# Kernel optimization log

Measured on AMD Instinct MI355X. Metric: run time of the kernel, lower is better.

The kernel has to match this reference:

```python
import jax, jax.numpy as jnp
import numpy as np

N_NODES = 50000
N_EDGES = 1600000
IN_DIM = 128
OUT_DIM = 32
N_HEADS = 4


def setup_inputs() -> dict:
    key = jax.random.key(0)
    k_x, k_e, k_w, k_a = jax.random.split(key, 4)
    x = jax.random.normal(k_x, (N_NODES, IN_DIM), dtype=jnp.float32)
    edge_index = jax.random.randint(k_e, (N_EDGES, 2), 0, N_NODES, dtype=jnp.int64)
    # Xavier-uniform-like init scales
    w_bound = np.sqrt(6.0 / (IN_DIM + OUT_DIM)).astype(np.float32)
    a_bound = np.sqrt(6.0 / (N_HEADS + 2 * OUT_DIM)).astype(np.float32)
    weight = jax.random.uniform(k_w, (N_HEADS, IN_DIM, OUT_DIM), dtype=jnp.float32,
                                minval=-w_bound, maxval=w_bound)
    attn = jax.random.uniform(k_a, (N_HEADS, 2 * OUT_DIM), dtype=jnp.float32,
                              minval=-a_bound, maxval=a_bound)
    return {"x": x, "edge_index": edge_index, "weight": weight, "attn": attn}


def reference(x, edge_index, weight, attn):
    # x: [N, in_dim]; edge_index: [E, 2]; weight: [H, in, out]; attn: [H, 2*out]
    num_nodes = x.shape[0]
    out_dim = weight.shape[2]
    src = edge_index[:, 0]
    dst = edge_index[:, 1]

    # Per-head linear transform: [N, H, out]
    Wh = jnp.einsum('ni,hio->nho', x, weight)
    Wh_src = Wh[src]  # [E, H, out]
    Wh_dst = Wh[dst]  # [E, H, out]

    a_src = attn[:, :out_dim]   # [H, out]
    a_dst = attn[:, out_dim:]   # [H, out]
    # Edge scores: [E, H]
    e = jnp.einsum('eho,ho->eh', Wh_src, a_src) + jnp.einsum('eho,ho->eh', Wh_dst, a_dst)
    e = jax.nn.leaky_relu(e, negative_slope=0.2)

    # Segment softmax over incoming edges of each dst node
    max_per_dst = jax.ops.segment_max(e, dst, num_segments=num_nodes)  # [N, H]
    max_per_dst = jnp.where(jnp.isfinite(max_per_dst), max_per_dst, 0.0)
    exp_e = jnp.exp(e - max_per_dst[dst])                               # [E, H]
    sum_per_dst = jax.ops.segment_sum(exp_e, dst, num_segments=num_nodes)  # [N, H]
    alpha = exp_e / (sum_per_dst[dst] + 1e-9)                           # [E, H]
    # Dropout is identity in eval mode.

    # Weighted scatter-add aggregation: [N, H, out]
    out = jax.ops.segment_sum(alpha[:, :, None] * Wh_src, dst, num_segments=num_nodes)
    h = out.reshape(num_nodes, -1)  # concat heads -> [N, H*out]
    return h, alpha
```

## Files before the change

### kernel.cpp

```cpp
#include <hip/hip_runtime.h>
#include <hip/hip_bf16.h>
#include <math.h>

#define N_NODES 50000
#define N_EDGES 1600000
#define IN_DIM  128
#define OUT_DIM 32
#define N_HEADS 4
#define WH_DIM  (N_HEADS * OUT_DIM)
#define CAP     128
#define NB_SCAN 196
#define NPASS   4
#define WIN     (N_NODES / NPASS)
#define NCH2    32
#define SEGCAP  420000
#define UNROLL  16
#define EPB     (256 * UNROLL)

typedef __attribute__((ext_vector_type(8))) short short8;
typedef __attribute__((ext_vector_type(4))) float floatx4;

__device__ __forceinline__ short f2bf(float v) {
    __hip_bfloat16 b = __float2bfloat16(v);
    return *reinterpret_cast<short*>(&b);
}
__device__ __forceinline__ float lrelu(float v) {
    return v > 0.0f ? v : 0.2f * v;
}

__device__ __forceinline__ void load_edge(const void* eidx, int is32, int e,
                                          int& s, int& d) {
    if (is32) {
        const int2 v = ((const int2*)eidx)[e];
        s = v.x; d = v.y;
    } else {
        const longlong2 v = ((const longlong2*)eidx)[e];
        s = (int)v.x; d = (int)v.y;
    }
}

__global__ __launch_bounds__(256) void k_prep(
        const float* __restrict__ weight, const float* __restrict__ attn,
        short* __restrict__ bsw_pre) {
    __shared__ float ubuf[128 * 8];
    const int t = threadIdx.x;
    {
        int c = t & 7, k0 = t >> 3;
        int h = c & 3;
        const float* ap = attn + h * 64 + (c >> 2) * 32;
        for (int k = k0; k < 128; k += 32) {
            const float* wp = weight + h * (IN_DIM * OUT_DIM) + k * OUT_DIM;
            float u = 0.f;
#pragma unroll
            for (int o = 0; o < 32; o += 4) {
                float4 wv = *(const float4*)(wp + o);
                float4 av = *(const float4*)(ap + o);
                u += wv.x * av.x + wv.y * av.y + wv.z * av.z + wv.w * av.w;
            }
            ubuf[k * 8 + c] = u;
        }
    }
    __syncthreads();
    for (int f = t; f < 128 * 128; f += 256) {
        int k = f >> 7, c = f & 127;
        float w = weight[(c >> 5) * (IN_DIM * OUT_DIM) + k * OUT_DIM + (c & 31)];
        int kc = k >> 5, quad = (k >> 3) & 3, j = k & 7;
        bsw_pre[((kc * 9 + (c >> 4)) * 64 + quad * 16 + (c & 15)) * 8 + j] =
            f2bf(w);
    }
    for (int f = t; f < 128 * 16; f += 256) {
        int k = f >> 4, c = f & 15;
        float w = (c < 8) ? ubuf[k * 8 + c] : 0.f;
        int kc = k >> 5, quad = (k >> 3) & 3, j = k & 7;
        bsw_pre[((kc * 9 + 8) * 64 + quad * 16 + c) * 8 + j] = f2bf(w);
    }
}

__global__ __launch_bounds__(256) void k_cvt(
        const void* __restrict__ eidx,
        int* __restrict__ win_cnt,
        int* __restrict__ win_s, int* __restrict__ win_d) {
    __shared__ int s_is32;
    __shared__ int wcnt[NPASS][UNROLL][4];
    __shared__ int pb[NPASS][UNROLL][4];
    __shared__ int bw[NPASS];
    const int t = threadIdx.x;
    const int wv = t >> 6, lane = t & 63;
    if (t < 64) {
        int hi = ((const int*)eidx)[2 * (t * 25000) + 1];
        unsigned long long b = __ballot(hi != 0);
        if (t == 0) s_is32 = (b != 0ULL) ? 1 : 0;
    }
    __syncthreads();
    const int is32 = s_is32;
    const int e0 = blockIdx.x * EPB;
    int sg[UNROLL], dg[UNROLL];
#pragma unroll
    for (int i = 0; i < UNROLL; ++i) {
        const int e = e0 + i * 256 + t;
        int s = 0, d = -1;
        if (e < N_EDGES) load_edge(eidx, is32, e, s, d);
        sg[i] = s; dg[i] = d;
        const int w = (d >= 0) ? (d / WIN) : -1;
        const unsigned long long m0 = __ballot(w == 0);
        const unsigned long long m1 = __ballot(w == 1);
        const unsigned long long m2 = __ballot(w == 2);
        const unsigned long long m3 = __ballot(w == 3);
        if (lane == 0) {
            wcnt[0][i][wv] = __popcll(m0);
            wcnt[1][i][wv] = __popcll(m1);
            wcnt[2][i][wv] = __popcll(m2);
            wcnt[3][i][wv] = __popcll(m3);
        }
    }
    __syncthreads();
    if (t < NPASS) {
        int run = 0;
        for (int i = 0; i < UNROLL; ++i)
            for (int v = 0; v < 4; ++v) {
                pb[t][i][v] = run;
                run += wcnt[t][i][v];
            }
        bw[t] = atomicAdd(&win_cnt[t], run);
    }
    __syncthreads();
    const unsigned long long mlt = (1ULL << lane) - 1ULL;
#pragma unroll
    for (int i = 0; i < UNROLL; ++i) {
        const int d = dg[i];
        const int w = (d >= 0) ? (d / WIN) : -1;
        const unsigned long long m0 = __ballot(w == 0);
        const unsigned long long m1 = __ballot(w == 1);
        const unsigned long long m2 = __ballot(w == 2);
        const unsigned long long m3 = __ballot(w == 3);
        if (w >= 0) {
            const unsigned long long mw = (w == 0) ? m0 : (w == 1) ? m1
                                        : (w == 2) ? m2 : m3;
            const int rank = __popcll(mw & mlt);
            const int p = bw[w] + pb[w][i][wv] + rank;
            if (p < SEGCAP) {
                win_s[w * SEGCAP + p] = sg[i];
                win_d[w * SEGCAP + p] = d;
            }
        }
    }
}

__global__ __launch_bounds__(256) void k_wh(
        const float* __restrict__ x, const short* __restrict__ bsw_pre,
        __hip_bfloat16* __restrict__ Wh16, float* __restrict__ sb16) {
    __shared__ short xsw[4 * 4 * 64 * 8];
    __shared__ short bsw[4 * 9 * 64 * 8];
    const int t  = threadIdx.x;
    const int nb = blockIdx.x * 64;

    for (int f = t; f < 4 * 9 * 64; f += 256)
        *(short8*)&bsw[f * 8] = *(const short8*)&bsw_pre[f * 8];
    for (int f = t; f < 64 * 32; f += 256) {
        int n = f >> 5, k = (f & 31) * 4;
        int ng = nb + n; if (ng > N_NODES - 1) ng = N_NODES - 1;
        float4 v = *(const float4*)(x + (size_t)ng * IN_DIM + k);
        int wg = n >> 4, m = n & 15, kc = k >> 5, quad = (k >> 3) & 3, j = k & 7;
        short4 sv = make_short4(f2bf(v.x), f2bf(v.y), f2bf(v.z), f2bf(v.w));
        *(short4*)&xsw[(((wg * 4 + kc) * 64) + quad * 16 + m) * 8 + j] = sv;
    }
    __syncthreads();

    const int wg = t >> 6, lane = t & 63;
    floatx4 acc[9];
#pragma unroll
    for (int i = 0; i < 9; ++i) acc[i] = (floatx4){0.f, 0.f, 0.f, 0.f};
#pragma unroll
    for (int kc = 0; kc < 4; ++kc) {
        short8 a = *(short8*)&xsw[((wg * 4 + kc) * 64 + lane) * 8];
#pragma unroll
        for (int cg = 0; cg < 9; ++cg) {
            short8 b = *(short8*)&bsw[((kc * 9 + cg) * 64 + lane) * 8];
            acc[cg] = __builtin_amdgcn_mfma_f32_16x16x32_bf16(a, b, acc[cg],
                                                              0, 0, 0);
        }
    }

    const int col = lane & 15, quad = lane >> 4;
#pragma unroll
    for (int r = 0; r < 4; ++r) {
        int n = nb + wg * 16 + quad * 4 + r;
        if (n >= N_NODES) continue;
#pragma unroll
        for (int cg = 0; cg < 8; ++cg)
            Wh16[(size_t)n * WH_DIM + cg * 16 + col] =
                __float2bfloat16(acc[cg][r]);
        if (col < 8) sb16[(size_t)n * 16 + col] = acc[8][r];
    }
}

__global__ __launch_bounds__(1024) void k_hist(
        const int* __restrict__ win_cnt, const int* __restrict__ win_d,
        int* __restrict__ hist) {
    __shared__ int hbin[WIN];
    const int c = blockIdx.x, w = blockIdx.y;
    for (int i = threadIdx.x; i < WIN; i += 1024) hbin[i] = 0;
    __syncthreads();
    const int cw = win_cnt[w];
    const int ce = (cw + NCH2 - 1) / NCH2;
    const int lo = c * ce;
    const int hi = min(lo + ce, cw);
    const int w0 = w * WIN;
    for (int i = lo + threadIdx.x; i < hi; i += 1024) {
        unsigned u = (unsigned)(win_d[w * SEGCAP + i] - w0);
        if (u < WIN) atomicAdd(&hbin[u], 1);
    }
    __syncthreads();
    for (int i = threadIdx.x; i < WIN; i += 1024)
        hist[(w * NCH2 + c) * WIN + i] = hbin[i];
}

__global__ __launch_bounds__(256) void k_scan1(
        const int* __restrict__ hist, int* __restrict__ pre,
        int* __restrict__ bsum) {
    __shared__ int sh[256];
    const int t = threadIdx.x;
    const int i = blockIdx.x * 256 + t;
    int v = 0;
    if (i < N_NODES) {
        const int w = i / WIN, bin = i % WIN;
        for (int c = 0; c < NCH2; ++c) v += hist[(w * NCH2 + c) * WIN + bin];
    }
    sh[t] = v;
    __syncthreads();
    for (int d = 1; d < 256; d <<= 1) {
        int u = (t >= d) ? sh[t - d] : 0;
        __syncthreads();
        sh[t] += u;
        __syncthreads();
    }
    if (i < N_NODES) pre[i] = sh[t] - v;
    if (t == 255) bsum[blockIdx.x] = sh[255];
}

__global__ __launch_bounds__(256) void k_base2(
        const int* __restrict__ bsum, const int* __restrict__ pre,
        int* __restrict__ hist, int* __restrict__ noff) {
    __shared__ int sh[256];
    const int t = threadIdx.x;
    int v = (t < NB_SCAN) ? bsum[t] : 0;
    sh[t] = v;
    __syncthreads();
    for (int d = 1; d < 256; d <<= 1) {
        int u = (t >= d) ? sh[t - d] : 0;
        __syncthreads();
        sh[t] += u;
        __syncthreads();
    }
    const int b = blockIdx.x;
    const int exb = sh[b] - bsum[b];
    if (b == 0 && t == 0) noff[N_NODES] = N_EDGES;
    const int i = b * 256 + t;
    if (i >= N_NODES) return;
    int run = pre[i] + exb;
    noff[i] = run;
    const int w = i / WIN, bin = i % WIN;
    for (int c = 0; c < NCH2; ++c) {
        const int idx = (w * NCH2 + c) * WIN + bin;
        int t0 = hist[idx];
        hist[idx] = run;
        run += t0;
    }
}

__global__ __launch_bounds__(1024) void k_scatter(
        const int* __restrict__ win_cnt, const int* __restrict__ win_s,
        const int* __restrict__ win_d,
        const int* __restrict__ hist, int* __restrict__ csr) {
    __shared__ int pos[WIN];
    const int c = blockIdx.x, w = blockIdx.y;
    for (int i = threadIdx.x; i < WIN; i += 1024)
        pos[i] = hist[(w * NCH2 + c) * WIN + i];
    __syncthreads();
    const int cw = win_cnt[w];
    const int ce = (cw + NCH2 - 1) / NCH2;
    const int lo = c * ce;
    const int hi = min(lo + ce, cw);
    const int w0 = w * WIN;
    for (int i = lo + threadIdx.x; i < hi; i += 1024) {
        int s = win_s[w * SEGCAP + i];
        unsigned u = (unsigned)(win_d[w * SEGCAP + i] - w0);
        if (u < WIN) {
            int p = atomicAdd(&pos[u], 1);
            csr[p] = s;
        }
    }
}

__global__ __launch_bounds__(256) void k_node(
        const int* __restrict__ noff,
        const int* __restrict__ csr, float* __restrict__ sb16,
        const __hip_bfloat16* __restrict__ Wh16,
        float* __restrict__ out_h) {
    __shared__ int    sbuf[4][CAP];
    __shared__ float4 e4b[4][CAP];
    const int wv = threadIdx.x >> 6;
    const int t  = threadIdx.x & 63;
    const int n  = blockIdx.x * 4 + wv;
    const int beg = noff[n];
    const int end = noff[n + 1];
    const int deg = end - beg;

    const float4 sd = *(const float4*)(sb16 + (size_t)n * 16 + 4);

    float4 sum = {0.f, 0.f, 0.f, 0.f};
    for (int l = t; l < deg; l += 64) {
        int s = csr[beg + l];
        float4 ss = *(const float4*)(sb16 + (size_t)s * 16);
        float4 ex;
        ex.x = __expf(lrelu(ss.x + sd.x));
        ex.y = __expf(lrelu(ss.y + sd.y));
        ex.z = __expf(lrelu(ss.z + sd.z));
        ex.w = __expf(lrelu(ss.w + sd.w));
        if (l < CAP) { sbuf[wv][l] = s; e4b[wv][l] = ex; }
        sum.x += ex.x; sum.y += ex.y; sum.z += ex.z; sum.w += ex.w;
    }
#pragma unroll
    for (int o = 32; o; o >>= 1) {
        sum.x += __shfl_xor(sum.x, o);
        sum.y += __shfl_xor(sum.y, o);
        sum.z += __shfl_xor(sum.z, o);
        sum.w += __shfl_xor(sum.w, o);
    }
    float4 inv;
    inv.x = 1.0f / (sum.x + 1e-9f); inv.y = 1.0f / (sum.y + 1e-9f);
    inv.z = 1.0f / (sum.z + 1e-9f); inv.w = 1.0f / (sum.w + 1e-9f);
    if (t == 0) *(float4*)(sb16 + (size_t)n * 16 + 8) = inv;

    const int esl = t >> 4;
    const int dsl = t & 15;
    const int h   = dsl >> 2;
    const float invh = (h == 0) ? inv.x : (h == 1) ? inv.y
                     : (h == 2) ? inv.z : inv.w;
    const float sdh  = (h == 0) ? sd.x : (h == 1) ? sd.y
                     : (h == 2) ? sd.z : sd.w;
    float acc0 = 0.f, acc1 = 0.f, acc2 = 0.f, acc3 = 0.f;
    float acc4 = 0.f, acc5 = 0.f, acc6 = 0.f, acc7 = 0.f;
    if (deg <= CAP) {
        const int sPad = sbuf[wv][0];
        for (int jb = 0; jb < deg; jb += 16) {
            int   sg[4];
            float ag[4];
#pragma unroll
            for (int g = 0; g < 4; ++g) {
                const int idx = jb + g * 4 + esl;
                sg[g] = sPad;
                ag[g] = 0.f;
                if (idx < deg) {
                    sg[g] = sbuf[wv][idx];
                    ag[g] = ((const float*)&e4b[wv][idx])[h];
                }
            }
            uint4 w0 = *(const uint4*)(Wh16 + (size_t)sg[0] * WH_DIM + dsl * 8);
            uint4 w1 = *(const uint4*)(Wh16 + (size_t)sg[1] * WH_DIM + dsl * 8);
            uint4 w2 = *(const uint4*)(Wh16 + (size_t)sg[2] * WH_DIM + dsl * 8);
            uint4 w3 = *(const uint4*)(Wh16 + (size_t)sg[3] * WH_DIM + dsl * 8);
#define ACC8(W, A)                                                            \
            acc0 += (A) * __uint_as_float((W).x << 16);                       \
            acc1 += (A) * __uint_as_float((W).x & 0xffff0000u);               \
            acc2 += (A) * __uint_as_float((W).y << 16);                       \
            acc3 += (A) * __uint_as_float((W).y & 0xffff0000u);               \
            acc4 += (A) * __uint_as_float((W).z << 16);                       \
            acc5 += (A) * __uint_as_float((W).z & 0xffff0000u);               \
            acc6 += (A) * __uint_as_float((W).w << 16);                       \
            acc7 += (A) * __uint_as_float((W).w & 0xffff0000u)
            ACC8(w0, ag[0]);
            ACC8(w1, ag[1]);
            ACC8(w2, ag[2]);
            ACC8(w3, ag[3]);
#undef ACC8
        }
    } else {
        for (int jb = 0; jb < deg; jb += 4) {
            const int idx = jb + esl;
            float a = 0.f;
            int s = sbuf[wv][0];
            if (idx < deg) {
                if (idx < CAP) {
                    s = sbuf[wv][idx];
                    a = ((const float*)&e4b[wv][idx])[h];
                } else {
                    s = csr[beg + idx];
                    a = __expf(lrelu(sb16[(size_t)s * 16 + h] + sdh));
                }
            }
            const uint4 w = *(const uint4*)(Wh16 + (size_t)s * WH_DIM + dsl * 8);
            acc0 += a * __uint_as_float(w.x << 16);
            acc1 += a * __uint_as_float(w.x & 0xffff0000u);
            acc2 += a * __uint_as_float(w.y << 16);
            acc3 += a * __uint_as_float(w.y & 0xffff0000u);
            acc4 += a * __uint_as_float(w.z << 16);
            acc5 += a * __uint_as_float(w.z & 0xffff0000u);
            acc6 += a * __uint_as_float(w.w << 16);
            acc7 += a * __uint_as_float(w.w & 0xffff0000u);
        }
    }
    acc0 += __shfl_xor(acc0, 16); acc0 += __shfl_xor(acc0, 32);
    acc1 += __shfl_xor(acc1, 16); acc1 += __shfl_xor(acc1, 32);
    acc2 += __shfl_xor(acc2, 16); acc2 += __shfl_xor(acc2, 32);
    acc3 += __shfl_xor(acc3, 16); acc3 += __shfl_xor(acc3, 32);
    acc4 += __shfl_xor(acc4, 16); acc4 += __shfl_xor(acc4, 32);
    acc5 += __shfl_xor(acc5, 16); acc5 += __shfl_xor(acc5, 32);
    acc6 += __shfl_xor(acc6, 16); acc6 += __shfl_xor(acc6, 32);
    acc7 += __shfl_xor(acc7, 16); acc7 += __shfl_xor(acc7, 32);
    if (t < 16) {
        float* op = out_h + (size_t)n * WH_DIM + dsl * 8;
        float4 o0 = {acc0 * invh, acc1 * invh, acc2 * invh, acc3 * invh};
        float4 o1 = {acc4 * invh, acc5 * invh, acc6 * invh, acc7 * invh};
        *(float4*)op = o0;
        *(float4*)(op + 4) = o1;
    }
}

__global__ __launch_bounds__(256) void k_alpha(
        const void* __restrict__ eidx,
        const float* __restrict__ sb16, float* __restrict__ ebuf) {
    __shared__ int s_is32;
    const int t = threadIdx.x;
    if (t < 64) {
        int hi = ((const int*)eidx)[2 * (t * 25000) + 1];
        unsigned long long b = __ballot(hi != 0);
        if (t == 0) s_is32 = (b != 0ULL) ? 1 : 0;
    }
    __syncthreads();
    const int e = blockIdx.x * 256 + t;
    int s, d;
    load_edge(eidx, s_is32, e, s, d);
    float4 ss = *(const float4*)(sb16 + (size_t)s * 16);
    float4 sd = *(const float4*)(sb16 + (size_t)d * 16 + 4);
    float4 iv = *(const float4*)(sb16 + (size_t)d * 16 + 8);
    float4 a;
    a.x = __expf(lrelu(ss.x + sd.x)) * iv.x;
    a.y = __expf(lrelu(ss.y + sd.y)) * iv.y;
    a.z = __expf(lrelu(ss.z + sd.z)) * iv.z;
    a.w = __expf(lrelu(ss.w + sd.w)) * iv.w;
    *(float4*)(ebuf + (size_t)e * 4) = a;
}

extern "C" void kernel_launch(void* const* d_in, const int* in_sizes, int n_in,
                              void* d_out, int out_size, void* d_ws, size_t ws_size,
                              hipStream_t stream) {
    const float* x      = (const float*)d_in[0];
    const void*  eidx   = d_in[1];
    const float* weight = (const float*)d_in[2];
    const float* attn   = (const float*)d_in[3];

    float* out   = (float*)d_out;
    float* out_h = out;
    float* ebuf  = out + (size_t)N_NODES * WH_DIM;

    char* ws = (char*)d_ws;
    int*   win_cnt = (int*)ws;
    int*   bsum    = (int*)(ws + 64);
    int*   pre     = (int*)(ws + 1024);
    int*   noff    = (int*)(ws + 201024);
    short* bsw_pre = (short*)(ws + 401088);
    int*   csr     = (int*)(ws + 13201088);
    int*   win_s   = (int*)(ws + 19601152);
    int*   win_d   = (int*)(ws + 26321152);
    int*   hist    = (int*)(ws + 33041152);
    __hip_bfloat16* Wh16 = (__hip_bfloat16*)(ws + 19601152);
    float* sb16    = (float*)(ws + 32401152);

    hipMemsetAsync(win_cnt, 0, 4 * sizeof(int), stream);

    k_prep<<<1, 256, 0, stream>>>(weight, attn, bsw_pre);
    k_cvt<<<(N_EDGES + EPB - 1) / EPB, 256, 0, stream>>>(eidx, win_cnt,
                                                         win_s, win_d);
    dim3 hg(NCH2, NPASS);
    k_hist<<<hg, 1024, 0, stream>>>(win_cnt, win_d, hist);
    k_scan1<<<NB_SCAN, 256, 0, stream>>>(hist, pre, bsum);
    k_base2<<<NB_SCAN, 256, 0, stream>>>(bsum, pre, hist, noff);
    k_scatter<<<hg, 1024, 0, stream>>>(win_cnt, win_s, win_d, hist, csr);
    k_wh<<<(N_NODES + 63) / 64, 256, 0, stream>>>(x, bsw_pre, Wh16, sb16);
    k_node<<<N_NODES / 4, 256, 0, stream>>>(noff, csr, sb16, Wh16, out_h);
    k_alpha<<<N_EDGES / 256, 256, 0, stream>>>(eidx, sb16, ebuf);
}
```

Baseline: 265.2 us.

## Fuse edge bucketing with Wh GEMM, pack src/dst, merge scan kernels

Merges the edge-window bucketing kernel and the MFMA Wh projection into one launch, with blocks split by index and shared memory overlaid through a union. Source and local destination are packed into one 32-bit word, which halves the bucket traffic read by the histogram and scatter passes. The two scan kernels become one that uses a flag-based spin on per-block sums, and the memset is folded into the prep kernel. This removes several launches and some memory traffic. The cost is a cross-block spin-wait that assumes all 196 scan blocks are resident at once, plus a 17-bit source field limit.

Measured after the change: 253.5 us. -4.4%, faster.

```diff
diff --git a/kernel.cpp b/kernel.cpp
--- a/kernel.cpp
+++ b/kernel.cpp
@@ -13,9 +13,12 @@
 #define NPASS   4
 #define WIN     (N_NODES / NPASS)
 #define NCH2    32
-#define SEGCAP  420000
+#define SEGCAP  410000
 #define UNROLL  16
 #define EPB     (256 * UNROLL)
+#define NB_CVT  391
+#define NB_WH   782
+#define SFLAG   (1 << 30)
 
 typedef __attribute__((ext_vector_type(8))) short short8;
 typedef __attribute__((ext_vector_type(4))) float floatx4;
@@ -39,11 +42,14 @@
     }
 }
 
-__global__ __launch_bounds__(256) void k_prep(
+__global__ __launch_bounds__(256) void k_prep0(
         const float* __restrict__ weight, const float* __restrict__ attn,
-        short* __restrict__ bsw_pre) {
+        short* __restrict__ bsw_pre, int* __restrict__ win_cnt,
+        int* __restrict__ bsum) {
     __shared__ float ubuf[128 * 8];
     const int t = threadIdx.x;
+    if (t < NPASS) win_cnt[t] = 0;
+    if (t < NB_SCAN) bsum[t] = 0;
     {
         int c = t & 7, k0 = t >> 3;
         int h = c & 3;
@@ -76,126 +82,130 @@
     }
 }
 
-__global__ __launch_bounds__(256) void k_cvt(
-        const void* __restrict__ eidx,
-        int* __restrict__ win_cnt,
-        int* __restrict__ win_s, int* __restrict__ win_d) {
-    __shared__ int s_is32;
-    __shared__ int wcnt[NPASS][UNROLL][4];
-    __shared__ int pb[NPASS][UNROLL][4];
-    __shared__ int bw[NPASS];
+union CvtWhSmem {
+    struct {
+        int s_is32;
+        int wcnt[NPASS][UNROLL][4];
+        int pb[NPASS][UNROLL][4];
+        int bw[NPASS];
+    } c;
+    struct {
+        short xsw[4 * 4 * 64 * 8];
+        short bsw[4 * 9 * 64 * 8];
+    } w;
+};
+
+__global__ __launch_bounds__(256) void k_cvtwh(
+        const void* __restrict__ eidx, const float* __restrict__ x,
+        const short* __restrict__ bsw_pre,
+        int* __restrict__ win_cnt, int* __restrict__ win_sd,
+        __hip_bfloat16* __restrict__ Wh16, float* __restrict__ sb16) {
+    __shared__ CvtWhSmem sm;
     const int t = threadIdx.x;
-    const int wv = t >> 6, lane = t & 63;
-    if (t < 64) {
-        int hi = ((const int*)eidx)[2 * (t * 25000) + 1];
-        unsigned long long b = __ballot(hi != 0);
-        if (t == 0) s_is32 = (b != 0ULL) ? 1 : 0;
-    }
-    __syncthreads();
-    const int is32 = s_is32;
-    const int e0 = blockIdx.x * EPB;
-    int sg[UNROLL], dg[UNROLL];
-#pragma unroll
-    for (int i = 0; i < UNROLL; ++i) {
-        const int e = e0 + i * 256 + t;
-        int s = 0, d = -1;
-        if (e < N_EDGES) load_edge(eidx, is32, e, s, d);
-        sg[i] = s; dg[i] = d;
-        const int w = (d >= 0) ? (d / WIN) : -1;
-        const unsigned long long m0 = __ballot(w == 0);
-        const unsigned long long m1 = __ballot(w == 1);
-        const unsigned long long m2 = __ballot(w == 2);
-        const unsigned long long m3 = __ballot(w == 3);
-        if (lane == 0) {
-            wcnt[0][i][wv] = __popcll(m0);
-            wcnt[1][i][wv] = __popcll(m1);
-            wcnt[2][i][wv] = __popcll(m2);
-            wcnt[3][i][wv] = __popcll(m3);
-        }
-    }
-    __syncthreads();
-    if (t < NPASS) {
-        int run = 0;
-        for (int i = 0; i < UNROLL; ++i)
-            for (int v = 0; v < 4; ++v) {
-                pb[t][i][v] = run;
-                run += wcnt[t][i][v];
-            }
-        bw[t] = atomicAdd(&win_cnt[t], run);
-    }
-    __syncthreads();
-    const unsigned long long mlt = (1ULL << lane) - 1ULL;
-#pragma unroll
-    for (int i = 0; i < UNROLL; ++i) {
-        const int d = dg[i];
-        const int w = (d >= 0) ? (d / WIN) : -1;
-        const unsigned long long m0 = __ballot(w == 0);
-        const unsigned long long m1 = __ballot(w == 1);
-        const unsigned long long m2 = __ballot(w == 2);
-        const unsigned long long m3 = __ballot(w == 3);
-        if (w >= 0) {
-            const unsigned long long mw = (w == 0) ? m0 : (w == 1) ? m1
-                                        : (w == 2) ? m2 : m3;
-            const int rank = __popcll(mw & mlt);
-            const int p = bw[w] + pb[w][i][wv] + rank;
-            if (p < SEGCAP) {
-                win_s[w * SEGCAP + p] = sg[i];
-                win_d[w * SEGCAP + p] = d;
-            }
-        }
-    }
-}
-
-__global__ __launch_bounds__(256) void k_wh(
-        const float* __restrict__ x, const short* __restrict__ bsw_pre,
-        __hip_bfloat16* __restrict__ Wh16, float* __restrict__ sb16) {
-    __shared__ short xsw[4 * 4 * 64 * 8];
-    __shared__ short bsw[4 * 9 * 64 * 8];
-    const int t  = threadIdx.x;
-    const int nb = blockIdx.x * 64;
-
-    for (int f = t; f < 4 * 9 * 64; f += 256)
-        *(short8*)&bsw[f * 8] = *(const short8*)&bsw_pre[f * 8];
-    for (int f = t; f < 64 * 32; f += 256) {
-        int n = f >> 5, k = (f & 31) * 4;
-        int ng = nb + n; if (ng > N_NODES - 1) ng = N_NODES - 1;
-        float4 v = *(const float4*)(x + (size_t)ng * IN_DIM + k);
-        int wg = n >> 4, m = n & 15, kc = k >> 5, quad = (k >> 3) & 3, j = k & 7;
-        short4 sv = make_short4(f2bf(v.x), f2bf(v.y), f2bf(v.z), f2bf(v.w));
-        *(short4*)&xsw[(((wg * 4 + kc) * 64) + quad * 16 + m) * 8 + j] = sv;
-    }
-    __syncthreads();
-
-    const int wg = t >> 6, lane = t & 63;
-    floatx4 acc[9];
-#pragma unroll
-    for (int i = 0; i < 9; ++i) acc[i] = (floatx4){0.f, 0.f, 0.f, 0.f};
-#pragma unroll
-    for (int kc = 0; kc < 4; ++kc) {
-        short8 a = *(short8*)&xsw[((wg * 4 + kc) * 64 + lane) * 8];
-#pragma unroll
-        for (int cg = 0; cg < 9; ++cg) {
-            short8 b = *(short8*)&bsw[((kc * 9 + cg) * 64 + lane) * 8];
-            acc[cg] = __builtin_amdgcn_mfma_f32_16x16x32_bf16(a, b, acc[cg],
-                                                              0, 0, 0);
-        }
-    }
-
-    const int col = lane & 15, quad = lane >> 4;
-#pragma unroll
-    for (int r = 0; r < 4; ++r) {
-        int n = nb + wg * 16 + quad * 4 + r;
-        if (n >= N_NODES) continue;
-#pragma unroll
-        for (int cg = 0; cg < 8; ++cg)
-            Wh16[(size_t)n * WH_DIM + cg * 16 + col] =
-                __float2bfloat16(acc[cg][r]);
-        if (col < 8) sb16[(size_t)n * 16 + col] = acc[8][r];
+
+    if (blockIdx.x < NB_CVT) {
+        const int wv = t >> 6, lane = t & 63;
+        if (t < 64) {
+            int hi = ((const int*)eidx)[2 * (t * 25000) + 1];
+            unsigned long long b = __ballot(hi != 0);
+            if (t == 0) sm.c.s_is32 = (b != 0ULL) ? 1 : 0;
+        }
+        __syncthreads();
+        const int is32 = sm.c.s_is32;
+        const int e0 = blockIdx.x * EPB;
+        int sg[UNROLL], dg[UNROLL];
+#pragma unroll
+        for (int i = 0; i < UNROLL; ++i) {
+            const int e = e0 + i * 256 + t;
+            int s = 0, d = -1;
+            if (e < N_EDGES) load_edge(eidx, is32, e, s, d);
+            sg[i] = s; dg[i] = d;
+            const int w = (d >= 0) ? (d / WIN) : -1;
+            const unsigned long long m0 = __ballot(w == 0);
+            const unsigned long long m1 = __ballot(w == 1);
+            const unsigned long long m2 = __ballot(w == 2);
+            const unsigned long long m3 = __ballot(w == 3);
+            if (lane == 0) {
+                sm.c.wcnt[0][i][wv] = __popcll(m0);
+                sm.c.wcnt[1][i][wv] = __popcll(m1);
+                sm.c.wcnt[2][i][wv] = __popcll(m2);
+                sm.c.wcnt[3][i][wv] = __popcll(m3);
+            }
+        }
+        __syncthreads();
+        if (t < NPASS) {
+            int run = 0;
+            for (int i = 0; i < UNROLL; ++i)
+                for (int v = 0; v < 4; ++v) {
+                    sm.c.pb[t][i][v] = run;
+                    run += sm.c.wcnt[t][i][v];
+                }
+            sm.c.bw[t] = atomicAdd(&win_cnt[t], run);
+        }
+        __syncthreads();
+        const unsigned long long mlt = (1ULL << lane) - 1ULL;
+#pragma unroll
+        for (int i = 0; i < UNROLL; ++i) {
+            const int d = dg[i];
+            const int w = (d >= 0) ? (d / WIN) : -1;
+            const unsigned long long m0 = __ballot(w == 0);
+            const unsigned long long m1 = __ballot(w == 1);
+            const unsigned long long m2 = __ballot(w == 2);
+            const unsigned long long m3 = __ballot(w == 3);
+            if (w >= 0) {
+                const unsigned long long mw = (w == 0) ? m0 : (w == 1) ? m1
+                                            : (w == 2) ? m2 : m3;
+                const int rank = __popcll(mw & mlt);
+                const int p = sm.c.bw[w] + sm.c.pb[w][i][wv] + rank;
+                if (p < SEGCAP)
+                    win_sd[w * SEGCAP + p] = sg[i] | ((d - w * WIN) << 17);
+            }
+        }
+    } else {
+        const int nb = (blockIdx.x - NB_CVT) * 64;
+        for (int f = t; f < 4 * 9 * 64; f += 256)
+            *(short8*)&sm.w.bsw[f * 8] = *(const short8*)&bsw_pre[f * 8];
+        for (int f = t; f < 64 * 32; f += 256) {
+            int n = f >> 5, k = (f & 31) * 4;
+            int ng = nb + n; if (ng > N_NODES - 1) ng = N_NODES - 1;
+            float4 v = *(const float4*)(x + (size_t)ng * IN_DIM + k);
+            int wg = n >> 4, m = n & 15, kc = k >> 5, quad = (k >> 3) & 3,
+                j = k & 7;
+            short4 sv = make_short4(f2bf(v.x), f2bf(v.y), f2bf(v.z), f2bf(v.w));
+            *(short4*)&sm.w.xsw[(((wg * 4 + kc) * 64) + quad * 16 + m) * 8 + j]
+                = sv;
+        }
+        __syncthreads();
+        const int wg = t >> 6, lane = t & 63;
+        floatx4 acc[9];
+#pragma unroll
+        for (int i = 0; i < 9; ++i) acc[i] = (floatx4){0.f, 0.f, 0.f, 0.f};
+#pragma unroll
+        for (int kc = 0; kc < 4; ++kc) {
+            short8 a = *(short8*)&sm.w.xsw[((wg * 4 + kc) * 64 + lane) * 8];
+#pragma unroll
+            for (int cg = 0; cg < 9; ++cg) {
+                short8 b = *(short8*)&sm.w.bsw[((kc * 9 + cg) * 64 + lane) * 8];
+                acc[cg] = __builtin_amdgcn_mfma_f32_16x16x32_bf16(a, b, acc[cg],
+                                                                  0, 0, 0);
+            }
+        }
+        const int col = lane & 15, quad = lane >> 4;
+#pragma unroll
+        for (int r = 0; r < 4; ++r) {
+            int n = nb + wg * 16 + quad * 4 + r;
+            if (n >= N_NODES) continue;
+#pragma unroll
+            for (int cg = 0; cg < 8; ++cg)
+                Wh16[(size_t)n * WH_DIM + cg * 16 + col] =
+                    __float2bfloat16(acc[cg][r]);
+            if (col < 8) sb16[(size_t)n * 16 + col] = acc[8][r];
+        }
     }
 }
 
 __global__ __launch_bounds__(1024) void k_hist(
-        const int* __restrict__ win_cnt, const int* __restrict__ win_d,
+        const int* __restrict__ win_cnt, const int* __restrict__ win_sd,
         int* __restrict__ hist) {
     __shared__ int hbin[WIN];
     const int c = blockIdx.x, w = blockIdx.y;
@@ -205,9 +215,8 @@
     const int ce = (cw + NCH2 - 1) / NCH2;
     const int lo = c * ce;
     const int hi = min(lo + ce, cw);
-    const int w0 = w * WIN;
     for (int i = lo + threadIdx.x; i < hi; i += 1024) {
-        unsigned u = (unsigned)(win_d[w * SEGCAP + i] - w0);
+        unsigned u = ((unsigned)win_sd[w * SEGCAP + i]) >> 17;
         if (u < WIN) atomicAdd(&hbin[u], 1);
     }
     __syncthreads();
@@ -215,12 +224,13 @@
         hist[(w * NCH2 + c) * WIN + i] = hbin[i];
 }
 
-__global__ __launch_bounds__(256) void k_scan1(
-        const int* __restrict__ hist, int* __restrict__ pre,
-        int* __restrict__ bsum) {
+__global__ __launch_bounds__(256) void k_scanbase(
+        int* __restrict__ bsum, int* __restrict__ hist,
+        int* __restrict__ noff) {
     __shared__ int sh[256];
     const int t = threadIdx.x;
-    const int i = blockIdx.x * 256 + t;
+    const int b = blockIdx.x;
+    const int i = b * 256 + t;
     int v = 0;
     if (i < N_NODES) {
         const int w = i / WIN, bin = i % WIN;
@@ -234,17 +244,16 @@
         sh[t] += u;
         __syncthreads();
     }
-    if (i < N_NODES) pre[i] = sh[t] - v;
-    if (t == 255) bsum[blockIdx.x] = sh[255];
-}
-
-__global__ __launch_bounds__(256) void k_base2(
-        const int* __restrict__ bsum, const int* __restrict__ pre,
-        int* __restrict__ hist, int* __restrict__ noff) {
-    __shared__ int sh[256];
-    const int t = threadIdx.x;
-    int v = (t < NB_SCAN) ? bsum[t] : 0;
-    sh[t] = v;
+    const int myex = sh[t] - v;
+    if (t == 255) atomicExch(&bsum[b], sh[255] | SFLAG);
+    __syncthreads();
+    int bvv = 0;
+    if (t < NB_SCAN) {
+        int xx;
+        do { xx = atomicAdd(&bsum[t], 0); } while (!(xx & SFLAG));
+        bvv = xx & ~SFLAG;
+    }
+    sh[t] = bvv;
     __syncthreads();
     for (int d = 1; d < 256; d <<= 1) {
         int u = (t >= d) ? sh[t - d] : 0;
@@ -252,12 +261,10 @@
         sh[t] += u;
         __syncthreads();
     }
-    const int b = blockIdx.x;
-    const int exb = sh[b] - bsum[b];
+    const int exb = (b == 0) ? 0 : sh[b - 1];
     if (b == 0 && t == 0) noff[N_NODES] = N_EDGES;
-    const int i = b * 256 + t;
     if (i >= N_NODES) return;
-    int run = pre[i] + exb;
+    int run = myex + exb;
     noff[i] = run;
     const int w = i / WIN, bin = i % WIN;
     for (int c = 0; c < NCH2; ++c) {
@@ -269,8 +276,7 @@
 }
 
 __global__ __launch_bounds__(1024) void k_scatter(
-        const int* __restrict__ win_cnt, const int* __restrict__ win_s,
-        const int* __restrict__ win_d,
+        const int* __restrict__ win_cnt, const int* __restrict__ win_sd,
         const int* __restrict__ hist, int* __restrict__ csr) {
     __shared__ int pos[WIN];
     const int c = blockIdx.x, w = blockIdx.y;
@@ -281,10 +287,10 @@
     const int ce = (cw + NCH2 - 1) / NCH2;
     const int lo = c * ce;
     const int hi = min(lo + ce, cw);
-    const int w0 = w * WIN;
     for (int i = lo + threadIdx.x; i < hi; i += 1024) {
-        int s = win_s[w * SEGCAP + i];
-        unsigned u = (unsigned)(win_d[w * SEGCAP + i] - w0);
+        const int pk = win_sd[w * SEGCAP + i];
+        const int s = pk & 0x1FFFF;
+        const unsigned u = ((unsigned)pk) >> 17;
         if (u < WIN) {
             int p = atomicAdd(&pos[u], 1);
             csr[p] = s;
@@ -457,27 +463,21 @@
     char* ws = (char*)d_ws;
     int*   win_cnt = (int*)ws;
     int*   bsum    = (int*)(ws + 64);
-    int*   pre     = (int*)(ws + 1024);
-    int*   noff    = (int*)(ws + 201024);
-    short* bsw_pre = (short*)(ws + 401088);
-    int*   csr     = (int*)(ws + 13201088);
-    int*   win_s   = (int*)(ws + 19601152);
-    int*   win_d   = (int*)(ws + 26321152);
-    int*   hist    = (int*)(ws + 33041152);
-    __hip_bfloat16* Wh16 = (__hip_bfloat16*)(ws + 19601152);
-    float* sb16    = (float*)(ws + 32401152);
-
-    hipMemsetAsync(win_cnt, 0, 4 * sizeof(int), stream);
-
-    k_prep<<<1, 256, 0, stream>>>(weight, attn, bsw_pre);
-    k_cvt<<<(N_EDGES + EPB - 1) / EPB, 256, 0, stream>>>(eidx, win_cnt,
-                                                         win_s, win_d);
+    short* bsw_pre = (short*)(ws + 1024);
+    int*   noff    = (int*)(ws + 37952);
+    int*   win_sd  = (int*)(ws + 238016);
+    int*   hist    = (int*)(ws + 6798080);
+    int*   csr     = (int*)(ws + 13198144);
+    __hip_bfloat16* Wh16 = (__hip_bfloat16*)(ws + 19598208);
+    float* sb16    = (float*)(ws + 32398272);
+
+    k_prep0<<<1, 256, 0, stream>>>(weight, attn, bsw_pre, win_cnt, bsum);
+    k_cvtwh<<<NB_CVT + NB_WH, 256, 0, stream>>>(eidx, x, bsw_pre, win_cnt,
+                                                win_sd, Wh16, sb16);
     dim3 hg(NCH2, NPASS);
-    k_hist<<<hg, 1024, 0, stream>>>(win_cnt, win_d, hist);
-    k_scan1<<<NB_SCAN, 256, 0, stream>>>(hist, pre, bsum);
-    k_base2<<<NB_SCAN, 256, 0, stream>>>(bsum, pre, hist, noff);
-    k_scatter<<<hg, 1024, 0, stream>>>(win_cnt, win_s, win_d, hist, csr);
-    k_wh<<<(N_NODES + 63) / 64, 256, 0, stream>>>(x, bsw_pre, Wh16, sb16);
+    k_hist<<<hg, 1024, 0, stream>>>(win_cnt, win_sd, hist);
+    k_scanbase<<<NB_SCAN, 256, 0, stream>>>(bsum, hist, noff);
+    k_scatter<<<hg, 1024, 0, stream>>>(win_cnt, win_sd, hist, csr);
     k_node<<<N_NODES / 4, 256, 0, stream>>>(noff, csr, sb16, Wh16, out_h);
     k_alpha<<<N_EDGES / 256, 256, 0, stream>>>(eidx, sb16, ebuf);
 }
```
